# Optimization experiments

Hardware: AMD Instinct MI355X
Metric: run time of the kernel (lower is better)

The kernel has to match this reference:

```python
import jax, jax.numpy as jnp
import numpy as np

D_MODEL = 1024
NUM_HEADS = 16


def setup_inputs() -> dict:
    key = jax.random.key(0)
    ks = jax.random.split(key, 5)
    B, N, D = 2, 2048, D_MODEL
    x = jax.random.normal(ks[0], (B, N, D), dtype=jnp.float32)
    Wq = jax.random.normal(ks[1], (D, D), dtype=jnp.float32) * 0.02
    Wk = jax.random.normal(ks[2], (D, D), dtype=jnp.float32) * 0.02
    Wv = jax.random.normal(ks[3], (D, D), dtype=jnp.float32) * 0.02
    Wo = jax.random.normal(ks[4], (D, D), dtype=jnp.float32) * 0.02
    return {"x": x, "Wq": Wq, "Wk": Wk, "Wv": Wv, "Wo": Wo}


def reference(x, Wq, Wk, Wv, Wo):
    # Executed path of QuantizedHyperbolicAttention.forward: TRITON_AVAILABLE is
    # False in the source, so the module always runs _pytorch_attention
    # (standard scaled-dot-product attention), mask=None.
    B, N, D = x.shape
    H = NUM_HEADS
    hd = D // H
    # nn.Linear(bias=False): y = x @ W.T
    q = (x @ Wq.T).reshape(B, N, H, hd).transpose(0, 2, 1, 3)  # [B,H,N,hd]
    k = (x @ Wk.T).reshape(B, N, H, hd).transpose(0, 2, 1, 3)
    v = (x @ Wv.T).reshape(B, N, H, hd).transpose(0, 2, 1, 3)
    scale = hd ** -0.5
    attn = jnp.einsum("bhnd,bhmd->bhnm", q, k) * scale  # [B,H,N,N]
    attn = jax.nn.softmax(attn, axis=-1)
    out = jnp.einsum("bhnm,bhmd->bhnd", attn, v)  # [B,H,N,hd]
    out = out.transpose(0, 2, 1, 3).reshape(B, N, D)
    return out @ Wo.T
```

## Files before the change

kernel.cpp:

```cpp
#include <hip/hip_runtime.h>

using u16 = unsigned short;
using u32 = unsigned int;

typedef __bf16 bf16x8 __attribute__((ext_vector_type(8)));
typedef float  f32x4  __attribute__((ext_vector_type(4)));
typedef float  f32x8  __attribute__((ext_vector_type(8)));
typedef float  f32x16 __attribute__((ext_vector_type(16)));
typedef u16    u16x8  __attribute__((ext_vector_type(8)));
typedef u32    u32x4  __attribute__((ext_vector_type(4)));

__device__ __forceinline__ u32 f2bf(float f) {
  u32 u = __builtin_bit_cast(u32, f);
  return (u + 0x7fffu + ((u >> 16) & 1u)) >> 16;
}

__device__ __forceinline__ void gload_lds16(const u16* g, u16* lds) {
  __builtin_amdgcn_global_load_lds(
      (const __attribute__((address_space(1))) void*)g,
      (__attribute__((address_space(3))) void*)lds, 16, 0, 0);
}

__device__ __forceinline__ u32 cvtpk(float lo, float hi) {
  u32 r;
  asm("v_cvt_pk_bf16_f32 %0, %1, %2" : "=v"(r) : "v"(lo), "v"(hi));
  return r;
}

__device__ __forceinline__ float xhalf_add(float v) {
  return v + __shfl_xor(v, 32);
}

__global__ __launch_bounds__(256) void cvt_all(
    const float* __restrict__ x,  const float* __restrict__ wq,
    const float* __restrict__ wk, const float* __restrict__ wv,
    const float* __restrict__ wo, u16* __restrict__ out) {
  size_t i = ((size_t)blockIdx.x * 256 + threadIdx.x) * 8;
  const float* src;
  if (i < 4194304) {
    src = x + i;
  } else {
    size_t j = i - 4194304;
    unsigned w = (unsigned)(j >> 20);
    size_t o = j & 1048575;
    src = (w == 0) ? (wq + o) : (w == 1) ? (wk + o) : (w == 2) ? (wv + o) : (wo + o);
  }
  f32x4 a = *(const f32x4*)src;
  f32x4 b = *(const f32x4*)(src + 4);
  u32x4 r;
  r[0] = f2bf(a[0]) | (f2bf(a[1]) << 16);
  r[1] = f2bf(a[2]) | (f2bf(a[3]) << 16);
  r[2] = f2bf(b[0]) | (f2bf(b[1]) << 16);
  r[3] = f2bf(b[2]) | (f2bf(b[3]) << 16);
  *(u32x4*)(out + i) = r;
}

template <bool F32OUT>
__device__ __forceinline__ void gemm_tile(const u16* __restrict__ A,
                                          const u16* __restrict__ Bm,
                                          void* __restrict__ Cv,
                                          int rowBase, int colBase, float scale) {
  __shared__ __align__(16) u16 As[128 * 64];
  __shared__ __align__(16) u16 Bs[128 * 64];

  const int t = threadIdx.x;
  const int lane = t & 63;
  const int wv = t >> 6;
  const int wr = (wv >> 1) * 64;
  const int wc = (wv & 1) * 64;
  const int l15 = lane & 15;
  const int lg = lane >> 4;

  f32x4 acc[4][4] = {};

  for (int kt = 0; kt < 1024; kt += 64) {
#pragma unroll
    for (int i = 0; i < 4; ++i) {
      int s = i * 256 + t;
      int row = s >> 3;
      int k2 = (s & 7) ^ (row & 7);
      const u16* ga = A  + (size_t)(rowBase + row) * 1024 + kt + k2 * 8;
      const u16* gb = Bm + (size_t)(colBase + row) * 1024 + kt + k2 * 8;
      gload_lds16(ga, &As[(i * 256 + wv * 64) * 8]);
      gload_lds16(gb, &Bs[(i * 256 + wv * 64) * 8]);
    }
    __syncthreads();
#pragma unroll
    for (int kk = 0; kk < 2; ++kk) {
      bf16x8 af[4], bfr[4];
#pragma unroll
      for (int m = 0; m < 4; ++m) {
        int row = wr + m * 16 + l15;
        af[m] = *(const bf16x8*)&As[row * 64 + (((kk * 4 + lg) ^ (row & 7)) * 8)];
      }
#pragma unroll
      for (int n = 0; n < 4; ++n) {
        int row = wc + n * 16 + l15;
        bfr[n] = *(const bf16x8*)&Bs[row * 64 + (((kk * 4 + lg) ^ (row & 7)) * 8)];
      }
      __builtin_amdgcn_s_setprio(1);
#pragma unroll
      for (int m = 0; m < 4; ++m)
#pragma unroll
        for (int n = 0; n < 4; ++n)
          acc[m][n] = __builtin_amdgcn_mfma_f32_16x16x32_bf16(af[m], bfr[n], acc[m][n], 0, 0, 0);
      __builtin_amdgcn_s_setprio(0);
    }
    __syncthreads();
  }

#pragma unroll
  for (int m = 0; m < 4; ++m) {
#pragma unroll
    for (int r = 0; r < 4; ++r) {
      int row = rowBase + wr + m * 16 + lg * 4 + r;
#pragma unroll
      for (int n = 0; n < 4; ++n) {
        int col = colBase + wc + n * 16 + l15;
        float v = acc[m][n][r] * scale;
        if (F32OUT)
          ((float*)Cv)[(size_t)row * 1024 + col] = v;
        else
          ((u16*)Cv)[(size_t)row * 1024 + col] = (u16)f2bf(v);
      }
    }
  }
}

__global__ __launch_bounds__(256) void gemm_qkv(
    const u16* __restrict__ xb,
    const u16* __restrict__ wq, const u16* __restrict__ wk, const u16* __restrict__ wv,
    u16* __restrict__ Qm, u16* __restrict__ Km, u16* __restrict__ Vm) {
  int bx = blockIdx.x;
  int mat = bx >> 8;
  int rem = bx & 255;
  int bm = rem & 31, bn = rem >> 5;
  const u16* B = (mat == 0) ? wq : (mat == 1) ? wk : wv;
  u16* C = (mat == 0) ? Qm : (mat == 1) ? Km : Vm;
  float scale = (mat == 0) ? 0.125f : 1.0f;
  gemm_tile<false>(xb, B, C, bm * 128, bn * 128, scale);
}

__global__ __launch_bounds__(256) void gemm_out(
    const u16* __restrict__ ao, const u16* __restrict__ wo, float* __restrict__ C) {
  int bm = blockIdx.x & 31, bn = blockIdx.x >> 5;
  gemm_tile<true>(ao, wo, C, bm * 128, bn * 128, 1.0f);
}

__global__ __launch_bounds__(512, 2) void attn_fwd(
    const u16* __restrict__ Q, const u16* __restrict__ K,
    const u16* __restrict__ V, u16* __restrict__ AO) {
  __shared__ __align__(16) u16 Ks[2][2][64 * 64];
  __shared__ __align__(16) u16 Vt[2][2][64 * 64];

  const int t = threadIdx.x;
  const int lane = t & 63;
  const int wv = t >> 6;
  const int wg = wv & 3;
  const int grp = wv >> 2;
  const int tg = t & 255;
  const int l31 = lane & 31;
  const int hi = lane >> 5;

  const int qb = blockIdx.x;
  const int pr = blockIdx.y;
  const size_t hb = (size_t)(pr >> 4) * 2048 * 1024 + (size_t)(pr & 15) * 64;
  const u16* Qh = Q + hb;
  const u16* Kh = K + hb;
  const u16* Vh = V + hb;
  u16* AOh = AO + hb;

  const int q0w = qb * 128 + wg * 32;
  const int kvb = grp * 1024;

  bf16x8 qf[4];
#pragma unroll
  for (int kk = 0; kk < 4; ++kk)
    qf[kk] = *(const bf16x8*)&Qh[(size_t)(q0w + l31) * 1024 + kk * 16 + hi * 8];

  f32x16 ot[2] = {};
  f32x8  Lacc = {};

  const int kv0 = (tg >> 3) * 2, d0 = (tg & 7) * 8;
  const int kxor = l31 & 7;
  const int kd0 = (l31 & 7) ^ (l31 >> 3);
  const int vg = (kv0 >> 4) * 2 + ((kv0 >> 2) & 1);
  const int vj = (kv0 & 3) + ((kv0 >> 3) & 1) * 4;

  {
#pragma unroll
    for (int i = 0; i < 2; ++i) {
      int s = i * 256 + tg;
      int row = s >> 3;
      int k2 = (s & 7) ^ (row & 7);
      gload_lds16(&Kh[(size_t)(kvb + row) * 1024 + k2 * 8],
                  &Ks[grp][0][(i * 256 + wg * 64) * 8]);
    }
    u16x8 v0 = *(const u16x8*)&Vh[(size_t)(kvb + kv0) * 1024 + d0];
    u16x8 v1 = *(const u16x8*)&Vh[(size_t)(kvb + kv0 + 1) * 1024 + d0];
#pragma unroll
    for (int e = 0; e < 8; ++e) {
      int d = d0 + e;
      int key = ((d & 7) ^ (d >> 3)) & 7;
      int idx = d * 64 + ((vg ^ key) * 8) + vj;
      *(u32*)&Vt[grp][0][idx] = (u32)v0[e] | ((u32)v1[e] << 16);
    }
  }
  __syncthreads();

  int cur = 0;
  for (int kt = kvb; kt < kvb + 1024; kt += 64) {
    u16x8 pv0, pv1;
    const bool pf = (kt + 64) < (kvb + 1024);
    if (pf) {
#pragma unroll
      for (int i = 0; i < 2; ++i) {
        int s = i * 256 + tg;
        int row = s >> 3;
        int k2 = (s & 7) ^ (row & 7);
        gload_lds16(&Kh[(size_t)(kt + 64 + row) * 1024 + k2 * 8],
                    &Ks[grp][cur ^ 1][(i * 256 + wg * 64) * 8]);
      }
      pv0 = *(const u16x8*)&Vh[(size_t)(kt + 64 + kv0) * 1024 + d0];
      pv1 = *(const u16x8*)&Vh[(size_t)(kt + 64 + kv0 + 1) * 1024 + d0];
    }

    const u16* ks = &Ks[grp][cur][0];
    f32x16 sc[2] = {};
#pragma unroll
    for (int kk = 0; kk < 4; ++kk) {
      bf16x8 kf0 = *(const bf16x8*)&ks[l31 * 64 + (((kk * 2 + hi) ^ kxor) * 8)];
      bf16x8 kf1 = *(const bf16x8*)&ks[(32 + l31) * 64 + (((kk * 2 + hi) ^ kxor) * 8)];
      __builtin_amdgcn_s_setprio(1);
      sc[0] = __builtin_amdgcn_mfma_f32_32x32x16_bf16(kf0, qf[kk], sc[0], 0, 0, 0);
      sc[1] = __builtin_amdgcn_mfma_f32_32x32x16_bf16(kf1, qf[kk], sc[1], 0, 0, 0);
      __builtin_amdgcn_s_setprio(0);
    }

#pragma unroll
    for (int fi = 0; fi < 2; ++fi)
#pragma unroll
      for (int r = 0; r < 16; ++r)
        sc[fi][r] = __expf(sc[fi][r]);
    {
      f32x8 lo0 = __builtin_shufflevector(sc[0], sc[0], 0,1,2,3,4,5,6,7);
      f32x8 hi0 = __builtin_shufflevector(sc[0], sc[0], 8,9,10,11,12,13,14,15);
      f32x8 lo1 = __builtin_shufflevector(sc[1], sc[1], 0,1,2,3,4,5,6,7);
      f32x8 hi1 = __builtin_shufflevector(sc[1], sc[1], 8,9,10,11,12,13,14,15);
      Lacc += (lo0 + hi0) + (lo1 + hi1);
    }

    bf16x8 pa[4];
#pragma unroll
    for (int fi = 0; fi < 2; ++fi) {
      u32x4 w0 = {cvtpk(sc[fi][0],  sc[fi][1]),  cvtpk(sc[fi][2],  sc[fi][3]),
                  cvtpk(sc[fi][4],  sc[fi][5]),  cvtpk(sc[fi][6],  sc[fi][7])};
      u32x4 w1 = {cvtpk(sc[fi][8],  sc[fi][9]),  cvtpk(sc[fi][10], sc[fi][11]),
                  cvtpk(sc[fi][12], sc[fi][13]), cvtpk(sc[fi][14], sc[fi][15])};
      pa[2 * fi]     = __builtin_bit_cast(bf16x8, w0);
      pa[2 * fi + 1] = __builtin_bit_cast(bf16x8, w1);
    }

    const u16* vt = &Vt[grp][cur][0];
#pragma unroll
    for (int kk = 0; kk < 4; ++kk) {
      bf16x8 vf0 = *(const bf16x8*)&vt[l31 * 64 + (((kk * 2 + hi) ^ kd0) * 8)];
      bf16x8 vf1 = *(const bf16x8*)&vt[(32 + l31) * 64 + (((kk * 2 + hi) ^ (kd0 ^ 4)) * 8)];
      __builtin_amdgcn_s_setprio(1);
      ot[0] = __builtin_amdgcn_mfma_f32_32x32x16_bf16(vf0, pa[kk], ot[0], 0, 0, 0);
      ot[1] = __builtin_amdgcn_mfma_f32_32x32x16_bf16(vf1, pa[kk], ot[1], 0, 0, 0);
      __builtin_amdgcn_s_setprio(0);
    }

    if (pf) {
#pragma unroll
      for (int e = 0; e < 8; ++e) {
        int d = d0 + e;
        int key = ((d & 7) ^ (d >> 3)) & 7;
        int idx = d * 64 + ((vg ^ key) * 8) + vj;
        *(u32*)&Vt[grp][cur ^ 1][idx] = (u32)pv0[e] | ((u32)pv1[e] << 16);
      }
    }
    __syncthreads();
    cur ^= 1;
  }

  float lp = (((Lacc[0] + Lacc[1]) + (Lacc[2] + Lacc[3])) +
              ((Lacc[4] + Lacc[5]) + (Lacc[6] + Lacc[7])));

  float* Osh = (float*)&Ks[0][0][0];
  float* Lsh = (float*)&Vt[0][0][0];
  const int pair = wg;
  const int obase = (((pair * 2 + hi) * 32) + l31) * 32;
  if (grp == 1) {
    *(f32x16*)&Osh[obase]      = ot[0];
    *(f32x16*)&Osh[obase + 16] = ot[1];
    Lsh[pair * 64 + lane] = lp;
  }
  __syncthreads();
  if (grp == 0) {
    ot[0] += *(const f32x16*)&Osh[obase];
    ot[1] += *(const f32x16*)&Osh[obase + 16];
    lp += Lsh[pair * 64 + lane];
    float L = xhalf_add(lp);
    float inv = 1.f / L;
    const size_t qrow = (size_t)(q0w + l31) * 1024;
#pragma unroll
    for (int dn = 0; dn < 2; ++dn)
#pragma unroll
      for (int j = 0; j < 8; ++j) {
        int r = 2 * j;
        int d = 2 * (j & 1) + 8 * (j >> 1) + 4 * hi + 32 * dn;
        u32 w = cvtpk(ot[dn][r] * inv, ot[dn][r + 1] * inv);
        *(u32*)&AOh[qrow + d] = w;
      }
  }
}

extern "C" void kernel_launch(void* const* d_in, const int* in_sizes, int n_in,
                              void* d_out, int out_size, void* d_ws, size_t ws_size,
                              hipStream_t stream) {
  const float* x  = (const float*)d_in[0];
  const float* wq = (const float*)d_in[1];
  const float* wk = (const float*)d_in[2];
  const float* wv = (const float*)d_in[3];
  const float* wo = (const float*)d_in[4];

  u16* ws = (u16*)d_ws;
  u16* xb  = ws;
  u16* wqb = ws + 4194304;
  u16* wkb = ws + 5242880;
  u16* wvb = ws + 6291456;
  u16* wob = ws + 7340032;
  u16* Qm  = ws + 8388608;
  u16* Km  = ws + 12582912;
  u16* Vm  = ws + 16777216;
  u16* AOm = ws + 20971520;

  cvt_all<<<4096, 256, 0, stream>>>(x, wq, wk, wv, wo, ws);
  gemm_qkv<<<768, 256, 0, stream>>>(xb, wqb, wkb, wvb, Qm, Km, Vm);
  attn_fwd<<<dim3(16, 32), 512, 0, stream>>>(Qm, Km, Vm, AOm);
  gemm_out<<<256, 256, 0, stream>>>(AOm, wob, (float*)d_out);
}
```

Before: 125.6 us.

## Emit V pre-transposed and swizzled from QKV GEMM for direct LDS loads

The V projection epilogue now stages its tile in shared memory and writes V to global memory per head, transposed [d][kv] and pre-swizzled. The attention kernel can then fetch V tiles with direct global-to-LDS async loads, the same way it fetches K. This removes the register round trip and the per-element transposing LDS stores from the attention inner loop. In exchange the GEMM epilogue gets an extra LDS pass and a barrier, and the swizzle must match the read pattern exactly.

```diff
diff --git a/kernel.cpp b/kernel.cpp
--- a/kernel.cpp
+++ b/kernel.cpp
@@ -55,13 +55,14 @@
   *(u32x4*)(out + i) = r;
 }
 
-template <bool F32OUT>
+template <int MODE>
 __device__ __forceinline__ void gemm_tile(const u16* __restrict__ A,
                                           const u16* __restrict__ Bm,
                                           void* __restrict__ Cv,
                                           int rowBase, int colBase, float scale) {
-  __shared__ __align__(16) u16 As[128 * 64];
-  __shared__ __align__(16) u16 Bs[128 * 64];
+  __shared__ __align__(16) u16 S[2 * 128 * 64];
+  u16* As = S;
+  u16* Bs = S + 8192;
 
   const int t = threadIdx.x;
   const int lane = t & 63;
@@ -109,6 +110,43 @@
     __syncthreads();
   }
 
+  if (MODE == 2) {
+#pragma unroll
+    for (int m = 0; m < 4; ++m)
+#pragma unroll
+      for (int r = 0; r < 4; ++r) {
+        int kvl = wr + m * 16 + lg * 4 + r;
+#pragma unroll
+        for (int n = 0; n < 4; ++n) {
+          int dl = wc + n * 16 + l15;
+          int bidx = dl * 256 + ((((kvl >> 3) ^ (dl & 7)) << 4)) + ((kvl & 7) << 1);
+          *(u16*)((char*)S + bidx) = (u16)f2bf(acc[m][n][r]);
+        }
+      }
+    __syncthreads();
+    const int dl = t >> 1, half = t & 1;
+    const int key = dl & 7;
+    const int head = (rowBase >> 11) * 16 + (colBase >> 6) + (dl >> 6);
+    const int d = dl & 63;
+    const int key64 = ((d & 7) ^ (d >> 3)) & 7;
+    const int kvb = rowBase & 2047;
+    u16x8 in[8];
+#pragma unroll
+    for (int lc = 0; lc < 8; ++lc)
+      in[lc] = *(const u16x8*)((char*)S + dl * 256 + ((half * 8 + (lc ^ key)) << 4));
+    u16* outp = (u16*)Cv + (size_t)head * 131072 + (size_t)d * 2048 + kvb + half * 64;
+#pragma unroll
+    for (int G = 0; G < 8; ++G) {
+      u16x8 o = (G & 1)
+        ? __builtin_shufflevector(in[(G >> 1) * 2], in[(G >> 1) * 2 + 1],
+                                  4, 5, 6, 7, 12, 13, 14, 15)
+        : __builtin_shufflevector(in[(G >> 1) * 2], in[(G >> 1) * 2 + 1],
+                                  0, 1, 2, 3, 8, 9, 10, 11);
+      *(u16x8*)(outp + ((G ^ key64) << 3)) = o;
+    }
+    return;
+  }
+
 #pragma unroll
   for (int m = 0; m < 4; ++m) {
 #pragma unroll
@@ -118,7 +156,7 @@
       for (int n = 0; n < 4; ++n) {
         int col = colBase + wc + n * 16 + l15;
         float v = acc[m][n][r] * scale;
-        if (F32OUT)
+        if (MODE == 1)
           ((float*)Cv)[(size_t)row * 1024 + col] = v;
         else
           ((u16*)Cv)[(size_t)row * 1024 + col] = (u16)f2bf(v);
@@ -130,26 +168,25 @@
 __global__ __launch_bounds__(256) void gemm_qkv(
     const u16* __restrict__ xb,
     const u16* __restrict__ wq, const u16* __restrict__ wk, const u16* __restrict__ wv,
-    u16* __restrict__ Qm, u16* __restrict__ Km, u16* __restrict__ Vm) {
+    u16* __restrict__ Qm, u16* __restrict__ Km, u16* __restrict__ Vtg) {
   int bx = blockIdx.x;
   int mat = bx >> 8;
   int rem = bx & 255;
   int bm = rem & 31, bn = rem >> 5;
-  const u16* B = (mat == 0) ? wq : (mat == 1) ? wk : wv;
-  u16* C = (mat == 0) ? Qm : (mat == 1) ? Km : Vm;
-  float scale = (mat == 0) ? 0.125f : 1.0f;
-  gemm_tile<false>(xb, B, C, bm * 128, bn * 128, scale);
+  if (mat == 0)      gemm_tile<0>(xb, wq, Qm,  bm * 128, bn * 128, 0.125f);
+  else if (mat == 1) gemm_tile<0>(xb, wk, Km,  bm * 128, bn * 128, 1.0f);
+  else               gemm_tile<2>(xb, wv, Vtg, bm * 128, bn * 128, 1.0f);
 }
 
 __global__ __launch_bounds__(256) void gemm_out(
     const u16* __restrict__ ao, const u16* __restrict__ wo, float* __restrict__ C) {
   int bm = blockIdx.x & 31, bn = blockIdx.x >> 5;
-  gemm_tile<true>(ao, wo, C, bm * 128, bn * 128, 1.0f);
+  gemm_tile<1>(ao, wo, C, bm * 128, bn * 128, 1.0f);
 }
 
 __global__ __launch_bounds__(512, 2) void attn_fwd(
     const u16* __restrict__ Q, const u16* __restrict__ K,
-    const u16* __restrict__ V, u16* __restrict__ AO) {
+    const u16* __restrict__ Vtg, u16* __restrict__ AO) {
   __shared__ __align__(16) u16 Ks[2][2][64 * 64];
   __shared__ __align__(16) u16 Vt[2][2][64 * 64];
 
@@ -167,7 +204,7 @@
   const size_t hb = (size_t)(pr >> 4) * 2048 * 1024 + (size_t)(pr & 15) * 64;
   const u16* Qh = Q + hb;
   const u16* Kh = K + hb;
-  const u16* Vh = V + hb;
+  const u16* Vth = Vtg + (size_t)pr * 131072;
   u16* AOh = AO + hb;
 
   const int q0w = qb * 128 + wg * 32;
@@ -181,48 +218,35 @@
   f32x16 ot[2] = {};
   f32x8  Lacc = {};
 
-  const int kv0 = (tg >> 3) * 2, d0 = (tg & 7) * 8;
   const int kxor = l31 & 7;
   const int kd0 = (l31 & 7) ^ (l31 >> 3);
-  const int vg = (kv0 >> 4) * 2 + ((kv0 >> 2) & 1);
-  const int vj = (kv0 & 3) + ((kv0 >> 3) & 1) * 4;
-
-  {
-#pragma unroll
-    for (int i = 0; i < 2; ++i) {
-      int s = i * 256 + tg;
-      int row = s >> 3;
-      int k2 = (s & 7) ^ (row & 7);
-      gload_lds16(&Kh[(size_t)(kvb + row) * 1024 + k2 * 8],
-                  &Ks[grp][0][(i * 256 + wg * 64) * 8]);
-    }
-    u16x8 v0 = *(const u16x8*)&Vh[(size_t)(kvb + kv0) * 1024 + d0];
-    u16x8 v1 = *(const u16x8*)&Vh[(size_t)(kvb + kv0 + 1) * 1024 + d0];
-#pragma unroll
-    for (int e = 0; e < 8; ++e) {
-      int d = d0 + e;
-      int key = ((d & 7) ^ (d >> 3)) & 7;
-      int idx = d * 64 + ((vg ^ key) * 8) + vj;
-      *(u32*)&Vt[grp][0][idx] = (u32)v0[e] | ((u32)v1[e] << 16);
-    }
+
+#pragma unroll
+  for (int i = 0; i < 2; ++i) {
+    int s = i * 256 + tg;
+    int krow = s >> 3;
+    int k2 = (s & 7) ^ (krow & 7);
+    gload_lds16(&Kh[(size_t)(kvb + krow) * 1024 + k2 * 8],
+                &Ks[grp][0][(i * 256 + wg * 64) * 8]);
+    gload_lds16(&Vth[(size_t)(s >> 3) * 2048 + kvb + (s & 7) * 8],
+                &Vt[grp][0][(i * 256 + wg * 64) * 8]);
   }
   __syncthreads();
 
   int cur = 0;
   for (int kt = kvb; kt < kvb + 1024; kt += 64) {
-    u16x8 pv0, pv1;
     const bool pf = (kt + 64) < (kvb + 1024);
     if (pf) {
 #pragma unroll
       for (int i = 0; i < 2; ++i) {
         int s = i * 256 + tg;
-        int row = s >> 3;
-        int k2 = (s & 7) ^ (row & 7);
-        gload_lds16(&Kh[(size_t)(kt + 64 + row) * 1024 + k2 * 8],
+        int krow = s >> 3;
+        int k2 = (s & 7) ^ (krow & 7);
+        gload_lds16(&Kh[(size_t)(kt + 64 + krow) * 1024 + k2 * 8],
                     &Ks[grp][cur ^ 1][(i * 256 + wg * 64) * 8]);
-      }
-      pv0 = *(const u16x8*)&Vh[(size_t)(kt + 64 + kv0) * 1024 + d0];
-      pv1 = *(const u16x8*)&Vh[(size_t)(kt + 64 + kv0 + 1) * 1024 + d0];
+        gload_lds16(&Vth[(size_t)(s >> 3) * 2048 + kt + 64 + (s & 7) * 8],
+                    &Vt[grp][cur ^ 1][(i * 256 + wg * 64) * 8]);
+      }
     }
 
     const u16* ks = &Ks[grp][cur][0];
@@ -272,15 +296,6 @@
       __builtin_amdgcn_s_setprio(0);
     }
 
-    if (pf) {
-#pragma unroll
-      for (int e = 0; e < 8; ++e) {
-        int d = d0 + e;
-        int key = ((d & 7) ^ (d >> 3)) & 7;
-        int idx = d * 64 + ((vg ^ key) * 8) + vj;
-        *(u32*)&Vt[grp][cur ^ 1][idx] = (u32)pv0[e] | ((u32)pv1[e] << 16);
-      }
-    }
     __syncthreads();
     cur ^= 1;
   }
@@ -334,11 +349,11 @@
   u16* wob = ws + 7340032;
   u16* Qm  = ws + 8388608;
   u16* Km  = ws + 12582912;
-  u16* Vm  = ws + 16777216;
+  u16* Vtg = ws + 16777216;
   u16* AOm = ws + 20971520;
 
   cvt_all<<<4096, 256, 0, stream>>>(x, wq, wk, wv, wo, ws);
-  gemm_qkv<<<768, 256, 0, stream>>>(xb, wqb, wkb, wvb, Qm, Km, Vm);
-  attn_fwd<<<dim3(16, 32), 512, 0, stream>>>(Qm, Km, Vm, AOm);
+  gemm_qkv<<<768, 256, 0, stream>>>(xb, wqb, wkb, wvb, Qm, Km, Vtg);
+  attn_fwd<<<dim3(16, 32), 512, 0, stream>>>(Qm, Km, Vtg, AOm);
   gemm_out<<<256, 256, 0, stream>>>(AOm, wob, (float*)d_out);
 }
```

Result: slower. 136.8 us (+8.9%).

## Software-pipeline attention loop: overlap QK^T of next tile with PV of previous

Applied to the files above, without the earlier changes.

Restructures the attention inner loop into a software pipeline. Each step issues the K load two tiles ahead and the V load one tile ahead, runs PV for the previous tile, then exp/pack for the current tile and QK^T for the next, using a triple-buffered transposed-V LDS array and two P register sets. Explicit waitcnt, sched_barrier and s_barrier calls replace the per-iteration __syncthreads. The aim is to hide global-load latency and keep the MFMA units busy across stages, at the cost of more LDS and registers.

```diff
diff --git a/kernel.cpp b/kernel.cpp
--- a/kernel.cpp
+++ b/kernel.cpp
@@ -151,13 +151,13 @@
     const u16* __restrict__ Q, const u16* __restrict__ K,
     const u16* __restrict__ V, u16* __restrict__ AO) {
   __shared__ __align__(16) u16 Ks[2][2][64 * 64];
-  __shared__ __align__(16) u16 Vt[2][2][64 * 64];
+  __shared__ __align__(16) u16 Vt3[2][3][64 * 64];
 
   const int t = threadIdx.x;
   const int lane = t & 63;
-  const int wv = t >> 6;
-  const int wg = wv & 3;
-  const int grp = wv >> 2;
+  const int wvi = t >> 6;
+  const int wg = wvi & 3;
+  const int grp = wvi >> 2;
   const int tg = t & 255;
   const int l31 = lane & 31;
   const int hi = lane >> 5;
@@ -179,54 +179,42 @@
     qf[kk] = *(const bf16x8*)&Qh[(size_t)(q0w + l31) * 1024 + kk * 16 + hi * 8];
 
   f32x16 ot[2] = {};
+  f32x16 sc[2];
   f32x8  Lacc = {};
-
-  const int kv0 = (tg >> 3) * 2, d0 = (tg & 7) * 8;
+  bf16x8 pa0[4], pa1[4];
+
   const int kxor = l31 & 7;
   const int kd0 = (l31 & 7) ^ (l31 >> 3);
+  const int kv0 = (tg >> 3) * 2, d0 = (tg & 7) * 8;
   const int vg = (kv0 >> 4) * 2 + ((kv0 >> 2) & 1);
   const int vj = (kv0 & 3) + ((kv0 >> 3) & 1) * 4;
 
-  {
+  auto VLOAD = [&](int tile, u16x8& a, u16x8& b) {
+    a = *(const u16x8*)&Vh[(size_t)(kvb + tile * 64 + kv0) * 1024 + d0];
+    b = *(const u16x8*)&Vh[(size_t)(kvb + tile * 64 + kv0 + 1) * 1024 + d0];
+  };
+  auto KSTAGE = [&](int tile, int buf) {
 #pragma unroll
     for (int i = 0; i < 2; ++i) {
       int s = i * 256 + tg;
-      int row = s >> 3;
-      int k2 = (s & 7) ^ (row & 7);
-      gload_lds16(&Kh[(size_t)(kvb + row) * 1024 + k2 * 8],
-                  &Ks[grp][0][(i * 256 + wg * 64) * 8]);
-    }
-    u16x8 v0 = *(const u16x8*)&Vh[(size_t)(kvb + kv0) * 1024 + d0];
-    u16x8 v1 = *(const u16x8*)&Vh[(size_t)(kvb + kv0 + 1) * 1024 + d0];
+      int krow = s >> 3;
+      int k2 = (s & 7) ^ (krow & 7);
+      gload_lds16(&Kh[(size_t)(kvb + tile * 64 + krow) * 1024 + k2 * 8],
+                  &Ks[grp][buf][(i * 256 + wg * 64) * 8]);
+    }
+  };
+  auto VPACK = [&](u16x8 a, u16x8 b, u16* dst) {
 #pragma unroll
     for (int e = 0; e < 8; ++e) {
       int d = d0 + e;
       int key = ((d & 7) ^ (d >> 3)) & 7;
       int idx = d * 64 + ((vg ^ key) * 8) + vj;
-      *(u32*)&Vt[grp][0][idx] = (u32)v0[e] | ((u32)v1[e] << 16);
-    }
-  }
-  __syncthreads();
-
-  int cur = 0;
-  for (int kt = kvb; kt < kvb + 1024; kt += 64) {
-    u16x8 pv0, pv1;
-    const bool pf = (kt + 64) < (kvb + 1024);
-    if (pf) {
-#pragma unroll
-      for (int i = 0; i < 2; ++i) {
-        int s = i * 256 + tg;
-        int row = s >> 3;
-        int k2 = (s & 7) ^ (row & 7);
-        gload_lds16(&Kh[(size_t)(kt + 64 + row) * 1024 + k2 * 8],
-                    &Ks[grp][cur ^ 1][(i * 256 + wg * 64) * 8]);
-      }
-      pv0 = *(const u16x8*)&Vh[(size_t)(kt + 64 + kv0) * 1024 + d0];
-      pv1 = *(const u16x8*)&Vh[(size_t)(kt + 64 + kv0 + 1) * 1024 + d0];
-    }
-
-    const u16* ks = &Ks[grp][cur][0];
-    f32x16 sc[2] = {};
+      *(u32*)&dst[idx] = (u32)a[e] | ((u32)b[e] << 16);
+    }
+  };
+  auto QKT = [&](const u16* ks) {
+    sc[0] = f32x16{};
+    sc[1] = f32x16{};
 #pragma unroll
     for (int kk = 0; kk < 4; ++kk) {
       bf16x8 kf0 = *(const bf16x8*)&ks[l31 * 64 + (((kk * 2 + hi) ^ kxor) * 8)];
@@ -236,7 +224,19 @@
       sc[1] = __builtin_amdgcn_mfma_f32_32x32x16_bf16(kf1, qf[kk], sc[1], 0, 0, 0);
       __builtin_amdgcn_s_setprio(0);
     }
-
+  };
+  auto PV = [&](const u16* vt, const bf16x8* pa) {
+#pragma unroll
+    for (int kk = 0; kk < 4; ++kk) {
+      bf16x8 vf0 = *(const bf16x8*)&vt[l31 * 64 + (((kk * 2 + hi) ^ kd0) * 8)];
+      bf16x8 vf1 = *(const bf16x8*)&vt[(32 + l31) * 64 + (((kk * 2 + hi) ^ (kd0 ^ 4)) * 8)];
+      __builtin_amdgcn_s_setprio(1);
+      ot[0] = __builtin_amdgcn_mfma_f32_32x32x16_bf16(vf0, pa[kk], ot[0], 0, 0, 0);
+      ot[1] = __builtin_amdgcn_mfma_f32_32x32x16_bf16(vf1, pa[kk], ot[1], 0, 0, 0);
+      __builtin_amdgcn_s_setprio(0);
+    }
+  };
+  auto EXPPACK = [&](bf16x8* pa) {
 #pragma unroll
     for (int fi = 0; fi < 2; ++fi)
 #pragma unroll
@@ -249,8 +249,6 @@
       f32x8 hi1 = __builtin_shufflevector(sc[1], sc[1], 8,9,10,11,12,13,14,15);
       Lacc += (lo0 + hi0) + (lo1 + hi1);
     }
-
-    bf16x8 pa[4];
 #pragma unroll
     for (int fi = 0; fi < 2; ++fi) {
       u32x4 w0 = {cvtpk(sc[fi][0],  sc[fi][1]),  cvtpk(sc[fi][2],  sc[fi][3]),
@@ -260,36 +258,73 @@
       pa[2 * fi]     = __builtin_bit_cast(bf16x8, w0);
       pa[2 * fi + 1] = __builtin_bit_cast(bf16x8, w1);
     }
-
-    const u16* vt = &Vt[grp][cur][0];
-#pragma unroll
-    for (int kk = 0; kk < 4; ++kk) {
-      bf16x8 vf0 = *(const bf16x8*)&vt[l31 * 64 + (((kk * 2 + hi) ^ kd0) * 8)];
-      bf16x8 vf1 = *(const bf16x8*)&vt[(32 + l31) * 64 + (((kk * 2 + hi) ^ (kd0 ^ 4)) * 8)];
-      __builtin_amdgcn_s_setprio(1);
-      ot[0] = __builtin_amdgcn_mfma_f32_32x32x16_bf16(vf0, pa[kk], ot[0], 0, 0, 0);
-      ot[1] = __builtin_amdgcn_mfma_f32_32x32x16_bf16(vf1, pa[kk], ot[1], 0, 0, 0);
-      __builtin_amdgcn_s_setprio(0);
-    }
-
-    if (pf) {
-#pragma unroll
-      for (int e = 0; e < 8; ++e) {
-        int d = d0 + e;
-        int key = ((d & 7) ^ (d >> 3)) & 7;
-        int idx = d * 64 + ((vg ^ key) * 8) + vj;
-        *(u32*)&Vt[grp][cur ^ 1][idx] = (u32)pv0[e] | ((u32)pv1[e] << 16);
-      }
-    }
-    __syncthreads();
-    cur ^= 1;
-  }
+  };
+
+  int vm1 = 2, v0 = 0, vp1 = 1;
+  auto ROT = [&]() { int tmp = vm1; vm1 = v0; v0 = vp1; vp1 = tmp; };
+
+  {
+    u16x8 a, b;
+    VLOAD(0, a, b);
+    __builtin_amdgcn_sched_barrier(0);
+    KSTAGE(0, 0);
+    KSTAGE(1, 1);
+    VPACK(a, b, &Vt3[grp][0][0]);
+    asm volatile("s_waitcnt vmcnt(2)" ::: "memory");
+    asm volatile("s_waitcnt lgkmcnt(0)" ::: "memory");
+    __builtin_amdgcn_sched_barrier(0);
+    __builtin_amdgcn_s_barrier();
+    QKT(&Ks[grp][0][0]);
+    asm volatile("s_waitcnt lgkmcnt(0)" ::: "memory");
+    __builtin_amdgcn_sched_barrier(0);
+    __builtin_amdgcn_s_barrier();
+  }
+
+  for (int tp = 0; tp < 7; ++tp) {
+#pragma unroll
+    for (int sub = 0; sub < 2; ++sub) {
+      const int tt = 2 * tp + sub;
+      u16x8 a, b;
+      VLOAD(tt + 1, a, b);
+      __builtin_amdgcn_sched_barrier(0);
+      KSTAGE(tt + 2, sub);
+      if (tt >= 1) PV(&Vt3[grp][vm1][0], sub ? pa0 : pa1);
+      EXPPACK(sub ? pa1 : pa0);
+      asm volatile("s_waitcnt vmcnt(4)" ::: "memory");
+      QKT(&Ks[grp][sub ^ 1][0]);
+      VPACK(a, b, &Vt3[grp][vp1][0]);
+      asm volatile("s_waitcnt lgkmcnt(0)" ::: "memory");
+      __builtin_amdgcn_sched_barrier(0);
+      __builtin_amdgcn_s_barrier();
+      ROT();
+    }
+  }
+
+  {
+    u16x8 a, b;
+    VLOAD(15, a, b);
+    __builtin_amdgcn_sched_barrier(0);
+    PV(&Vt3[grp][vm1][0], pa1);
+    EXPPACK(pa0);
+    asm volatile("s_waitcnt vmcnt(2)" ::: "memory");
+    QKT(&Ks[grp][1][0]);
+    VPACK(a, b, &Vt3[grp][vp1][0]);
+    asm volatile("s_waitcnt lgkmcnt(0)" ::: "memory");
+    __builtin_amdgcn_sched_barrier(0);
+    __builtin_amdgcn_s_barrier();
+    ROT();
+  }
+  PV(&Vt3[grp][vm1][0], pa0);
+  EXPPACK(pa1);
+  ROT();
+  PV(&Vt3[grp][vm1][0], pa1);
 
   float lp = (((Lacc[0] + Lacc[1]) + (Lacc[2] + Lacc[3])) +
               ((Lacc[4] + Lacc[5]) + (Lacc[6] + Lacc[7])));
 
+  __syncthreads();
   float* Osh = (float*)&Ks[0][0][0];
-  float* Lsh = (float*)&Vt[0][0][0];
+  float* Lsh = (float*)&Vt3[0][0][0];
   const int pair = wg;
   const int obase = (((pair * 2 + hi) * 32) + l31) * 32;
   if (grp == 1) {
```

Result: faster. 112.7 us (-10.3%).
